# Kernel optimization log

Hardware: AMD Instinct MI355X
Metric: run time of the kernel (lower is better)

Reference implementation:

```python
import jax, jax.numpy as jnp
import numpy as np

B, S, E, H = 2, 2048, 1024, 16
DH = E // H


def setup_inputs() -> dict:
    key = jax.random.key(0)
    ks = jax.random.split(key, 9)
    s = 1.0 / np.sqrt(E)
    return {
        "queries": jax.random.normal(ks[0], (B, S, E), dtype=jnp.float32),
        "keys": jax.random.normal(ks[1], (B, S, E), dtype=jnp.float32),
        "values": jax.random.normal(ks[2], (B, S, E), dtype=jnp.float32),
        "mask": jax.random.randint(ks[3], (B, 1, 1, S), 0, 2, dtype=jnp.int32),
        "Wq": jax.random.normal(ks[4], (E, E), dtype=jnp.float32) * s,
        "Wk": jax.random.normal(ks[5], (E, E), dtype=jnp.float32) * s,
        "Wv": jax.random.normal(ks[6], (E, E), dtype=jnp.float32) * s,
        "Wo": jax.random.normal(ks[7], (E, E), dtype=jnp.float32) * s,
        "bo": jax.random.normal(ks[8], (E,), dtype=jnp.float32) * s,
    }


def reference(queries, keys, values, mask, Wq, Wk, Wv, Wo, bo):
    n, d_q, _ = queries.shape
    d_k = keys.shape[1]
    # Linear projections (torch Linear: x @ W.T), then split into heads
    q = (queries @ Wq.T).reshape(n, d_q, H, DH)
    k = (keys @ Wk.T).reshape(n, d_k, H, DH)
    v = (values @ Wv.T).reshape(n, d_k, H, DH)
    # [n, H, d_q, d_k] attention scores
    energy = jnp.einsum("nqhd,nkhd->nhqk", q, k)
    energy = jnp.where(mask == 0, jnp.float32(-1e20), energy)
    # NOTE: original scales by sqrt(key seq length), not head dim -- kept faithful
    attn = jax.nn.softmax(energy / jnp.sqrt(jnp.float32(d_k)), axis=3)
    out = jnp.einsum("nhql,nlhd->nqhd", attn, v).reshape(n, d_q, E)
    return out @ Wo.T + bo
```

## Files before the change

kernel.cpp:

```cpp
#include <hip/hip_runtime.h>
#include <hip/hip_bf16.h>

#define BB 2
#define SS 2048
#define EE 1024
#define HH 16
#define DHH 64

using bf16x8 = __attribute__((ext_vector_type(8))) __bf16;
using f32x4  = __attribute__((ext_vector_type(4))) float;
using f32x16 = __attribute__((ext_vector_type(16))) float;
using uint2v = __attribute__((ext_vector_type(2))) unsigned int;

#if __has_builtin(__builtin_amdgcn_exp2f)
#define EXP2(x) __builtin_amdgcn_exp2f(x)
#else
#define EXP2(x) __exp2f(x)
#endif

__device__ int g_nkeep[2];

static __device__ __forceinline__ unsigned short f2bf(float f) {
    unsigned int u = __float_as_uint(f);
    u += 0x7FFFu + ((u >> 16) & 1u);
    return (unsigned short)(u >> 16);
}

static __device__ __forceinline__ unsigned int pk2bf(float lo, float hi) {
    union { __hip_bfloat162 h2; unsigned int u; } c;
    c.h2 = __float22bfloat162_rn(float2{lo, hi});
    return c.u;
}

static __device__ __forceinline__ void async_load16(const void* g, void* l) {
    __builtin_amdgcn_global_load_lds(
        (const __attribute__((address_space(1))) unsigned int*)g,
        (__attribute__((address_space(3))) unsigned int*)l, 16, 0, 0);
}

__global__ void cvt_kernel(const float* __restrict__ W0, const float* __restrict__ W1,
                           const float* __restrict__ W2, const float* __restrict__ W3,
                           const int* __restrict__ mask,
                           unsigned short* __restrict__ Wb,
                           int* __restrict__ srcTab)
{
    const int z = blockIdx.y;
    if (z == 4) {
        if (blockIdx.x >= 2) return;
        __shared__ int wsum[4];
        const int b    = blockIdx.x;
        const int tid  = threadIdx.x;
        const int lane = tid & 63;
        const int wave = tid >> 6;

        const int base = tid * 8;
        int v[8]; int run = 0;
        #pragma unroll
        for (int i = 0; i < 8; i++) { v[i] = (mask[b * SS + base + i] != 0) ? 1 : 0; run += v[i]; }

        int inc = run;
        #pragma unroll
        for (int d = 1; d < 64; d <<= 1) {
            int n = __shfl_up(inc, d, 64);
            if (lane >= d) inc += n;
        }
        if (lane == 63) wsum[wave] = inc;

        #pragma unroll
        for (int i = 0; i < 8; i++) srcTab[b * SS + base + i] = -1;
        __syncthreads();

        const int nkeep = wsum[0] + wsum[1] + wsum[2] + wsum[3];
        if (tid == 0) g_nkeep[b] = nkeep;

        int r = inc - run;
        #pragma unroll
        for (int w = 0; w < 4; w++) if (w < wave) r += wsum[w];
        #pragma unroll
        for (int i = 0; i < 8; i++) {
            if (v[i]) { srcTab[b * SS + r] = base + i; r++; }
        }
        return;
    }

    const float* src = (z == 0) ? W0 : (z == 1) ? W1 : (z == 2) ? W2 : W3;
    unsigned short* dst = Wb + (size_t)z * 1048576;
    const size_t base = (size_t)blockIdx.x * 2048 + (size_t)threadIdx.x * 8;
    const float4 f0 = *(const float4*)(src + base);
    const float4 f1 = *(const float4*)(src + base + 4);
    uint4 p;
    p.x = pk2bf(f0.x, f0.y); p.y = pk2bf(f0.z, f0.w);
    p.z = pk2bf(f1.x, f1.y); p.w = pk2bf(f1.z, f1.w);
    *(uint4*)(dst + base) = p;
}

template<int MT, int NT, bool BF16OUT, int AMODE>
__global__ __launch_bounds__(256, 3)
void gemm_xwt(const unsigned short* __restrict__ Xb0, const unsigned short* __restrict__ Xb1,
              const unsigned short* __restrict__ Xb2,
              const float* __restrict__ Xf0, const float* __restrict__ Xf1,
              const float* __restrict__ Xf2, const int* __restrict__ srcTab,
              const unsigned short* __restrict__ W0, const unsigned short* __restrict__ W1,
              const unsigned short* __restrict__ W2,
              void* __restrict__ Y0, void* __restrict__ Y1, void* __restrict__ Y2,
              const float* __restrict__ bias, int M, int N, int K,
              float s0, float s1, float s2)
{
    constexpr int BK = 32;
    constexpr int NI = MT / 32;
    constexpr int NJ = NT / 32;
    constexpr int LPS0 = MT / 64 + NT / 64;
    __shared__ __align__(16) unsigned short As[3][MT * BK];
    __shared__ __align__(16) unsigned short Bs[3][NT * BK];

    const int z = blockIdx.z;
    const unsigned short* __restrict__ W = (z == 0) ? W0 : ((z == 1) ? W1 : W2);
    void* __restrict__ Y                 = (z == 0) ? Y0 : ((z == 1) ? Y1 : Y2);
    const float ysc                      = (z == 0) ? s0 : ((z == 1) ? s1 : s2);

    const int tid  = threadIdx.x;
    const int lane = tid & 63;
    const int wave = tid >> 6;
    const int wm   = (wave >> 1) * (MT / 2);
    const int wn   = (wave & 1) * (NT / 2);

    const unsigned gx  = gridDim.x;
    const unsigned lin = blockIdx.x + gx * blockIdx.y;
    const unsigned k8  = lin & 7u;
    const unsigned j   = lin >> 3;
    const int m0 = (int)(k8 + (j / gx) * 8u) * MT;
    const int n0 = (int)(j % gx) * NT;

    if (AMODE == 1 && z > 0) {
        const int bb = m0 >> 11;
        if ((m0 & 2047) >= g_nkeep[bb]) return;
    }

    const int l16  = lane & 15;
    const int quad = lane >> 4;

    const int arow = lane >> 2;
    const int akc  = ((lane & 3) ^ ((lane >> 3) & 3)) * 8;
    const int rchunk = (quad ^ ((l16 >> 1) & 3)) * 8;
    const int awc  = ((lane & 3) ^ ((arow >> 1) & 3)) * 8;

    f32x4 acc[NI][NJ];
    #pragma unroll
    for (int i = 0; i < NI; i++)
        #pragma unroll
        for (int j2 = 0; j2 < NJ; j2++) acc[i][j2] = f32x4{0.f, 0.f, 0.f, 0.f};

    auto stageB = [&](int k0, int buf) {
        #pragma unroll
        for (int j2 = 0; j2 < NT / 64; j2++) {
            const int rr = wave * (NT / 4) + j2 * 16;
            async_load16(W + (size_t)(n0 + rr + arow) * K + k0 + akc, Bs[buf] + rr * BK);
        }
    };

    auto compute = [&](int buf) {
        bf16x8 afrag[NI], bfrag[NJ];
        #pragma unroll
        for (int ii = 0; ii < NI; ii++)
            afrag[ii] = *(const bf16x8*)(As[buf] + (wm + ii * 16 + l16) * BK + rchunk);
        #pragma unroll
        for (int j2 = 0; j2 < NJ; j2++)
            bfrag[j2] = *(const bf16x8*)(Bs[buf] + (wn + j2 * 16 + l16) * BK + rchunk);
        #pragma unroll
        for (int ii = 0; ii < NI; ii++)
            #pragma unroll
            for (int j2 = 0; j2 < NJ; j2++)
                acc[ii][j2] = __builtin_amdgcn_mfma_f32_16x16x32_bf16(afrag[ii], bfrag[j2], acc[ii][j2], 0, 0, 0);
    };

    const int niter = K / BK;

    if constexpr (AMODE == 0) {
        const unsigned short* __restrict__ X = (z == 0) ? Xb0 : ((z == 1) ? Xb1 : Xb2);
        auto stageA0 = [&](int k0, int buf) {
            #pragma unroll
            for (int j2 = 0; j2 < MT / 64; j2++) {
                const int rr = wave * (MT / 4) + j2 * 16;
                async_load16(X + (size_t)(m0 + rr + arow) * K + k0 + akc, As[buf] + rr * BK);
            }
        };
        stageB(0, 0); stageA0(0, 0);
        stageB(BK, 1); stageA0(BK, 1);
        int cur = 0;
        for (int i = 0; i < niter; i++) {
            if (i + 1 < niter) {
                if constexpr (LPS0 == 4)      asm volatile("s_waitcnt vmcnt(4)" ::: "memory");
                else if constexpr (LPS0 == 3) asm volatile("s_waitcnt vmcnt(3)" ::: "memory");
                else                          asm volatile("s_waitcnt vmcnt(2)" ::: "memory");
            } else {
                asm volatile("s_waitcnt vmcnt(0)" ::: "memory");
            }
            __builtin_amdgcn_s_barrier();
            if (i + 2 < niter) {
                const int nb = (cur >= 1) ? cur - 1 : 2;
                stageB((i + 2) * BK, nb); stageA0((i + 2) * BK, nb);
            }
            compute(cur);
            cur = (cur < 2) ? cur + 1 : 0;
        }
    } else {
        const float* __restrict__ XF = (z == 0) ? Xf0 : ((z == 1) ? Xf1 : Xf2);
        const int bb   = m0 >> 11;
        const int mloc = m0 & 2047;

        const float* aptr[2];
        bool azero[2];
        #pragma unroll
        for (int j2 = 0; j2 < 2; j2++) {
            const int rloc = wave * (MT / 4) + j2 * 16 + arow;
            int grow;
            if (z == 0) {
                grow = m0 + rloc; azero[j2] = false;
            } else {
                const int s = srcTab[bb * SS + mloc + rloc];
                azero[j2] = (s < 0);
                grow = bb * SS + (azero[j2] ? 0 : s);
            }
            aptr[j2] = XF + (size_t)grow * K + (lane & 3) * 8;
        }

        float4 aS0[4], aS1[4];
        #define STAGE_A(k0, S)                                                \
            { _Pragma("unroll")                                               \
              for (int j2 = 0; j2 < 2; j2++) {                                \
                  S[j2 * 2]     = *(const float4*)(aptr[j2] + (k0));          \
                  S[j2 * 2 + 1] = *(const float4*)(aptr[j2] + (k0) + 4);      \
              } }
        #define WRITE_A(buf, S)                                               \
            { _Pragma("unroll")                                               \
              for (int j2 = 0; j2 < 2; j2++) {                                \
                  uint4 w;                                                    \
                  w.x = pk2bf(S[j2*2].x, S[j2*2].y);                          \
                  w.y = pk2bf(S[j2*2].z, S[j2*2].w);                          \
                  w.z = pk2bf(S[j2*2+1].x, S[j2*2+1].y);                      \
                  w.w = pk2bf(S[j2*2+1].z, S[j2*2+1].w);                      \
                  if (azero[j2]) w = uint4{0, 0, 0, 0};                       \
                  const int rr = wave * (MT / 4) + j2 * 16 + arow;            \
                  *(uint4*)(As[buf] + rr * BK + awc) = w;                     \
              } }

        STAGE_A(0, aS0);
        STAGE_A(BK, aS1);
        stageB(0, 0);
        asm volatile("s_waitcnt vmcnt(6)" ::: "memory");
        WRITE_A(0, aS0);
        STAGE_A(2 * BK, aS0);
        stageB(BK, 1);
        asm volatile("s_waitcnt lgkmcnt(0)" ::: "memory");
        asm volatile("s_waitcnt vmcnt(6)" ::: "memory");
        __builtin_amdgcn_s_barrier();

        for (int i = 0; i < niter; i += 2) {
            if (i + 1 < niter) WRITE_A((i + 1) % 3, aS1);
            if (i + 3 < niter) STAGE_A((i + 3) * BK, aS1);
            if (i + 2 < niter) stageB((i + 2) * BK, (i + 2) % 3);
            compute(i % 3);
            asm volatile("s_waitcnt lgkmcnt(0)" ::: "memory");
            if (i + 3 < niter) asm volatile("s_waitcnt vmcnt(6)" ::: "memory");
            else               asm volatile("s_waitcnt vmcnt(0)" ::: "memory");
            __builtin_amdgcn_s_barrier();

            if (i + 2 < niter) WRITE_A((i + 2) % 3, aS0);
            if (i + 4 < niter) STAGE_A((i + 4) * BK, aS0);
            if (i + 3 < niter) stageB((i + 3) * BK, (i + 3) % 3);
            compute((i + 1) % 3);
            if (i + 2 < niter) {
                asm volatile("s_waitcnt lgkmcnt(0)" ::: "memory");
                if (i + 4 < niter) asm volatile("s_waitcnt vmcnt(6)" ::: "memory");
                else               asm volatile("s_waitcnt vmcnt(0)" ::: "memory");
                __builtin_amdgcn_s_barrier();
            }
        }
        #undef STAGE_A
        #undef WRITE_A
    }

    if (BF16OUT && z == 2) {
        #pragma unroll
        for (int i = 0; i < NI; i++) {
            #pragma unroll
            for (int j2 = 0; j2 < NJ; j2++) {
                const int row  = m0 + wm + i * 16 + quad * 4;
                const int bb2  = row >> 11;
                const int slot = row & 2047;
                const int col  = n0 + wn + j2 * 16 + l16;
                uint2 pck;
                pck.x = pk2bf(acc[i][j2][0], acc[i][j2][1]);
                pck.y = pk2bf(acc[i][j2][2], acc[i][j2][3]);
                *(uint2*)((unsigned short*)Y + ((size_t)(bb2 * EE + col)) * SS + slot) = pck;
            }
        }
    } else {
        #pragma unroll
        for (int i = 0; i < NI; i++) {
            #pragma unroll
            for (int j2 = 0; j2 < NJ; j2++) {
                #pragma unroll
                for (int r = 0; r < 4; r++) {
                    const int row = m0 + wm + i * 16 + quad * 4 + r;
                    const int col = n0 + wn + j2 * 16 + l16;
                    const float v = acc[i][j2][r];
                    if (BF16OUT) {
                        ((unsigned short*)Y)[(size_t)row * N + col] = f2bf(v * ysc);
                    } else {
                        ((float*)Y)[(size_t)row * N + col] = v + bias[col];
                    }
                }
            }
        }
    }
}

__global__ __launch_bounds__(256, 2)
void attn_kernel(const unsigned short* __restrict__ Qb,
                 const unsigned short* __restrict__ Kc,
                 const unsigned short* __restrict__ Vtc,
                 const int* __restrict__ mask,
                 unsigned short* __restrict__ AO)
{
    constexpr int LDK = 68;
    constexpr int LDV = 68;
    __shared__ __align__(16) unsigned short Ks[64 * LDK];
    __shared__ __align__(16) unsigned short Vs[64 * LDV];
    __shared__ float Lsum[4][32];
    __shared__ int nk_s;

    const int tid  = threadIdx.x;
    const int lane = tid & 63;
    const int wave = tid >> 6;
    const int l32  = lane & 31;
    const int hi   = lane >> 5;

    const int linear = blockIdx.x;
    const int bh     = (linear & 7) * 4 + ((linear >> 3) & 3);
    const int qblk   = linear >> 5;
    const int b  = bh >> 4;
    const int h  = bh & 15;
    const int q0 = qblk * 128 + wave * 32;

    if (tid == 0) nk_s = 0;
    __syncthreads();
    {
        int cnt = 0;
        #pragma unroll
        for (int i = 0; i < 8; i++) cnt += (mask[b * SS + tid * 8 + i] != 0) ? 1 : 0;
        #pragma unroll
        for (int d = 32; d >= 1; d >>= 1) cnt += __shfl_xor(cnt, d, 64);
        if (lane == 0) atomicAdd(&nk_s, cnt);
    }
    __syncthreads();
    const int nkeep  = nk_s;
    const int ntiles = (nkeep + 63) >> 6;

    bf16x8 qf[4];
    {
        const unsigned short* qptr = Qb + (size_t)(b * SS + q0 + l32) * EE + h * DHH + hi * 8;
        #pragma unroll
        for (int t = 0; t < 4; t++) qf[t] = *(const bf16x8*)(qptr + t * 16);
    }

    float lsum = 0.f;
    f32x16 o_acc[2];
    #pragma unroll
    for (int d = 0; d < 2; d++)
        #pragma unroll
        for (int r = 0; r < 16; r++) o_acc[d][r] = 0.f;

    const int srow = tid >> 2;
    const int sc   = (tid & 3) * 16;

    uint4 kr0, kr1, vr0, vr1;
    auto gload = [&](int t0) {
        const unsigned short* kg = Kc + (size_t)(b * SS + t0 + srow) * EE + h * DHH + sc;
        kr0 = *(const uint4*)(kg);
        kr1 = *(const uint4*)(kg + 8);
        const unsigned short* vg = Vtc + (size_t)(b * EE + h * DHH + srow) * SS + t0 + sc;
        vr0 = *(const uint4*)(vg);
        vr1 = *(const uint4*)(vg + 8);
    };
    gload(0);

    for (int it = 0; it < ntiles; it++) {
        const int t0 = it * 64;
        __syncthreads();
        *(uint4*)(Ks + srow * LDK + sc)     = kr0;
        *(uint4*)(Ks + srow * LDK + sc + 8) = kr1;
        *(uint4*)(Vs + srow * LDV + sc)     = vr0;
        *(uint4*)(Vs + srow * LDV + sc + 8) = vr1;
        __syncthreads();

        if (it + 1 < ntiles) gload(t0 + 64);

        const bool full = (t0 + 64 <= nkeep);

        #pragma unroll
        for (int blk = 0; blk < 2; blk++) {
            f32x16 s;
            __builtin_amdgcn_s_setprio(1);
            {
                bf16x8 kf = *(const bf16x8*)(Ks + (blk * 32 + l32) * LDK + hi * 8);
                f32x16 z;
                #pragma unroll
                for (int r = 0; r < 16; r++) z[r] = 0.f;
                s = __builtin_amdgcn_mfma_f32_32x32x16_bf16(kf, qf[0], z, 0, 0, 0);
            }
            #pragma unroll
            for (int t = 1; t < 4; t++) {
                bf16x8 kf = *(const bf16x8*)(Ks + (blk * 32 + l32) * LDK + t * 16 + hi * 8);
                s = __builtin_amdgcn_mfma_f32_32x32x16_bf16(kf, qf[t], s, 0, 0, 0);
            }
            __builtin_amdgcn_s_setprio(0);

            float p[16];
            #pragma unroll
            for (int r = 0; r < 16; r++) p[r] = EXP2(s[r]);
            if (!full) {
                const int keyb = t0 + blk * 32 + 4 * hi;
                #pragma unroll
                for (int r = 0; r < 16; r++)
                    if (keyb + ((r & 3) + 8 * (r >> 2)) >= nkeep) p[r] = 0.f;
            }
            #pragma unroll
            for (int r = 0; r < 16; r += 4)
                lsum += ((p[r] + p[r + 1]) + (p[r + 2] + p[r + 3]));

            const unsigned int u0 = pk2bf(p[0],  p[1]);
            const unsigned int u1 = pk2bf(p[2],  p[3]);
            const unsigned int u2 = pk2bf(p[4],  p[5]);
            const unsigned int u3 = pk2bf(p[6],  p[7]);
            const unsigned int u4 = pk2bf(p[8],  p[9]);
            const unsigned int u5 = pk2bf(p[10], p[11]);
            const unsigned int u6 = pk2bf(p[12], p[13]);
            const unsigned int u7 = pk2bf(p[14], p[15]);
            const uint2v s02 = __builtin_amdgcn_permlane32_swap(u0, u2, false, false);
            const uint2v s13 = __builtin_amdgcn_permlane32_swap(u1, u3, false, false);
            const uint2v s46 = __builtin_amdgcn_permlane32_swap(u4, u6, false, false);
            const uint2v s57 = __builtin_amdgcn_permlane32_swap(u5, u7, false, false);

            union { unsigned int u[4]; bf16x8 v; } pa0, pa1;
            pa0.u[0] = s02.x; pa0.u[1] = s13.x; pa0.u[2] = s02.y; pa0.u[3] = s13.y;
            pa1.u[0] = s46.x; pa1.u[1] = s57.x; pa1.u[2] = s46.y; pa1.u[3] = s57.y;

            __builtin_amdgcn_s_setprio(1);
            #pragma unroll
            for (int kc = 0; kc < 2; kc++) {
                const bf16x8 pav = (kc == 0) ? pa0.v : pa1.v;
                #pragma unroll
                for (int dblk = 0; dblk < 2; dblk++) {
                    bf16x8 vf = *(const bf16x8*)(Vs + (dblk * 32 + l32) * LDV + blk * 32 + kc * 16 + hi * 8);
                    o_acc[dblk] = __builtin_amdgcn_mfma_f32_32x32x16_bf16(pav, vf, o_acc[dblk], 0, 0, 0);
                }
            }
            __builtin_amdgcn_s_setprio(0);
        }
    }

    {
        float ls = lsum;
        ls += __shfl_xor(ls, 32, 64);
        Lsum[wave][l32] = 1.0f / ls;
    }
    __builtin_amdgcn_s_waitcnt(0xC07F);

    #pragma unroll
    for (int r = 0; r < 16; r++) {
        const int qr = (r & 3) + 8 * (r >> 2) + 4 * hi;
        const float rl = Lsum[wave][qr];
        const size_t orow = (size_t)(b * SS + q0 + qr) * EE + h * DHH + l32;
        AO[orow]      = f2bf(o_acc[0][r] * rl);
        AO[orow + 32] = f2bf(o_acc[1][r] * rl);
    }
}

extern "C" void kernel_launch(void* const* d_in, const int* in_sizes, int n_in,
                              void* d_out, int out_size, void* d_ws, size_t ws_size,
                              hipStream_t stream)
{
    (void)in_sizes; (void)n_in; (void)out_size; (void)ws_size;
    const float* queries = (const float*)d_in[0];
    const float* keys    = (const float*)d_in[1];
    const float* values  = (const float*)d_in[2];
    const int*   mask    = (const int*)d_in[3];
    const float* Wq      = (const float*)d_in[4];
    const float* Wk      = (const float*)d_in[5];
    const float* Wv      = (const float*)d_in[6];
    const float* Wo      = (const float*)d_in[7];
    const float* bo      = (const float*)d_in[8];

    const size_t NE = (size_t)BB * SS * EE;
    const size_t WE = (size_t)EE * EE;

    unsigned short* Wb  = (unsigned short*)d_ws;
    unsigned short* Qb  = Wb + 4 * WE;
    unsigned short* Kc  = Qb + NE;
    unsigned short* Vtc = Kc + NE;
    unsigned short* AOb = Vtc + NE;

    int* srcTab = (int*)d_out;

    const int M = BB * SS, N = EE, K = EE;
    const float qscale = 0.022097086912079608f * 1.4426950408889634f;

    cvt_kernel<<<dim3(512, 5), 256, 0, stream>>>(
        Wq, Wk, Wv, Wo, mask, Wb, srcTab);

    dim3 gproj(N / 128, M / 128, 3);
    gemm_xwt<128, 128, true, 1><<<gproj, 256, 0, stream>>>(
        nullptr, nullptr, nullptr,
        queries, keys, values, srcTab,
        Wb, Wb + WE, Wb + 2 * WE,
        (void*)Qb, (void*)Kc, (void*)Vtc, nullptr, M, N, K,
        qscale, 1.0f, 1.0f);

    attn_kernel<<<dim3(512), 256, 0, stream>>>(Qb, Kc, Vtc, mask, AOb);

    dim3 gout(N / 64, M / 64, 1);
    gemm_xwt<64, 64, false, 0><<<gout, 256, 0, stream>>>(
        AOb, AOb, AOb,
        nullptr, nullptr, nullptr, nullptr,
        Wb + 3 * WE, Wb + 3 * WE, Wb + 3 * WE,
        d_out, d_out, d_out, bo, M, N, K, 1.0f, 1.0f, 1.0f);
}
```

Before: 205.4 us.

## Use intra-block split-K with 512 threads for output projection GEMM

The output projection GEMM now uses 128x64 tiles with 512 threads, where two groups of four waves each handle half of the K dimension with separate triple-buffered LDS stages. At the end the halves are reduced through shared memory. The block-to-tile swizzle is also changed so that the eight-block groups stride across M. The aim is more waves per tile for latency hiding and better reuse of the larger A tile. The cost is extra LDS use, a reduction step and an additional barrier.

```diff
diff --git a/kernel.cpp b/kernel.cpp
--- a/kernel.cpp
+++ b/kernel.cpp
@@ -94,8 +94,8 @@
     *(uint4*)(dst + base) = p;
 }
 
-template<int MT, int NT, bool BF16OUT, int AMODE>
-__global__ __launch_bounds__(256, 3)
+template<int MT, int NT, bool BF16OUT, int AMODE, int NTH = 256>
+__global__ __launch_bounds__(NTH, NTH == 256 ? 3 : 4)
 void gemm_xwt(const unsigned short* __restrict__ Xb0, const unsigned short* __restrict__ Xb1,
               const unsigned short* __restrict__ Xb2,
               const float* __restrict__ Xf0, const float* __restrict__ Xf1,
@@ -109,9 +109,11 @@
     constexpr int BK = 32;
     constexpr int NI = MT / 32;
     constexpr int NJ = NT / 32;
+    constexpr bool SPLITK = (NTH == 512);
+    constexpr int NBUF = SPLITK ? 6 : 3;
     constexpr int LPS0 = MT / 64 + NT / 64;
-    __shared__ __align__(16) unsigned short As[3][MT * BK];
-    __shared__ __align__(16) unsigned short Bs[3][NT * BK];
+    __shared__ __align__(16) unsigned short As[NBUF][MT * BK];
+    __shared__ __align__(16) unsigned short Bs[NBUF][NT * BK];
 
     const int z = blockIdx.z;
     const unsigned short* __restrict__ W = (z == 0) ? W0 : ((z == 1) ? W1 : W2);
@@ -121,14 +123,17 @@
     const int tid  = threadIdx.x;
     const int lane = tid & 63;
     const int wave = tid >> 6;
-    const int wm   = (wave >> 1) * (MT / 2);
-    const int wn   = (wave & 1) * (NT / 2);
+    const int kh   = SPLITK ? (wave >> 2) : 0;
+    const int wq   = SPLITK ? (wave & 3) : wave;
+    const int wm   = (wq >> 1) * (MT / 2);
+    const int wn   = (wq & 1) * (NT / 2);
 
     const unsigned gx  = gridDim.x;
+    const unsigned gy  = gridDim.y;
     const unsigned lin = blockIdx.x + gx * blockIdx.y;
     const unsigned k8  = lin & 7u;
     const unsigned j   = lin >> 3;
-    const int m0 = (int)(k8 + (j / gx) * 8u) * MT;
+    const int m0 = (int)(k8 * (gy >> 3) + j / gx) * MT;
     const int n0 = (int)(j % gx) * NT;
 
     if (AMODE == 1 && z > 0) {
@@ -150,22 +155,22 @@
         #pragma unroll
         for (int j2 = 0; j2 < NJ; j2++) acc[i][j2] = f32x4{0.f, 0.f, 0.f, 0.f};
 
-    auto stageB = [&](int k0, int buf) {
+    auto stageB = [&](int k0, int bufAbs) {
         #pragma unroll
         for (int j2 = 0; j2 < NT / 64; j2++) {
-            const int rr = wave * (NT / 4) + j2 * 16;
-            async_load16(W + (size_t)(n0 + rr + arow) * K + k0 + akc, Bs[buf] + rr * BK);
+            const int rr = wq * (NT / 4) + j2 * 16;
+            async_load16(W + (size_t)(n0 + rr + arow) * K + k0 + akc, Bs[bufAbs] + rr * BK);
         }
     };
 
-    auto compute = [&](int buf) {
+    auto compute = [&](int bufAbs) {
         bf16x8 afrag[NI], bfrag[NJ];
         #pragma unroll
         for (int ii = 0; ii < NI; ii++)
-            afrag[ii] = *(const bf16x8*)(As[buf] + (wm + ii * 16 + l16) * BK + rchunk);
+            afrag[ii] = *(const bf16x8*)(As[bufAbs] + (wm + ii * 16 + l16) * BK + rchunk);
         #pragma unroll
         for (int j2 = 0; j2 < NJ; j2++)
-            bfrag[j2] = *(const bf16x8*)(Bs[buf] + (wn + j2 * 16 + l16) * BK + rchunk);
+            bfrag[j2] = *(const bf16x8*)(Bs[bufAbs] + (wn + j2 * 16 + l16) * BK + rchunk);
         #pragma unroll
         for (int ii = 0; ii < NI; ii++)
             #pragma unroll
@@ -173,19 +178,21 @@
                 acc[ii][j2] = __builtin_amdgcn_mfma_f32_16x16x32_bf16(afrag[ii], bfrag[j2], acc[ii][j2], 0, 0, 0);
     };
 
-    const int niter = K / BK;
-
     if constexpr (AMODE == 0) {
         const unsigned short* __restrict__ X = (z == 0) ? Xb0 : ((z == 1) ? Xb1 : Xb2);
-        auto stageA0 = [&](int k0, int buf) {
+        auto stageA0 = [&](int k0, int bufAbs) {
             #pragma unroll
             for (int j2 = 0; j2 < MT / 64; j2++) {
-                const int rr = wave * (MT / 4) + j2 * 16;
-                async_load16(X + (size_t)(m0 + rr + arow) * K + k0 + akc, As[buf] + rr * BK);
+                const int rr = wq * (MT / 4) + j2 * 16;
+                async_load16(X + (size_t)(m0 + rr + arow) * K + k0 + akc, As[bufAbs] + rr * BK);
             }
         };
-        stageB(0, 0); stageA0(0, 0);
-        stageB(BK, 1); stageA0(BK, 1);
+        const int kbase = SPLITK ? kh * (K / 2) : 0;
+        const int niter = (SPLITK ? K / 2 : K) / BK;
+        const int bof   = kh * 3;
+
+        stageB(kbase, bof + 0); stageA0(kbase, bof + 0);
+        stageB(kbase + BK, bof + 1); stageA0(kbase + BK, bof + 1);
         int cur = 0;
         for (int i = 0; i < niter; i++) {
             if (i + 1 < niter) {
@@ -198,12 +205,37 @@
             __builtin_amdgcn_s_barrier();
             if (i + 2 < niter) {
                 const int nb = (cur >= 1) ? cur - 1 : 2;
-                stageB((i + 2) * BK, nb); stageA0((i + 2) * BK, nb);
-            }
-            compute(cur);
+                stageB(kbase + (i + 2) * BK, bof + nb); stageA0(kbase + (i + 2) * BK, bof + nb);
+            }
+            compute(bof + cur);
             cur = (cur < 2) ? cur + 1 : 0;
         }
+
+        if constexpr (SPLITK) {
+            __syncthreads();
+            float* red = (float*)&As[0][0];
+            const int slot = ((wq * 64 + lane) * (NI * NJ * 4));
+            if (kh == 1) {
+                #pragma unroll
+                for (int i = 0; i < NI; i++)
+                    #pragma unroll
+                    for (int j2 = 0; j2 < NJ; j2++)
+                        #pragma unroll
+                        for (int r = 0; r < 4; r++)
+                            red[slot + (i * NJ + j2) * 4 + r] = acc[i][j2][r];
+            }
+            __syncthreads();
+            if (kh == 1) return;
+            #pragma unroll
+            for (int i = 0; i < NI; i++)
+                #pragma unroll
+                for (int j2 = 0; j2 < NJ; j2++)
+                    #pragma unroll
+                    for (int r = 0; r < 4; r++)
+                        acc[i][j2][r] += red[slot + (i * NJ + j2) * 4 + r];
+        }
     } else {
+        const int niter = K / BK;
         const float* __restrict__ XF = (z == 0) ? Xf0 : ((z == 1) ? Xf1 : Xf2);
         const int bb   = m0 >> 11;
         const int mloc = m0 & 2047;
@@ -212,7 +244,7 @@
         bool azero[2];
         #pragma unroll
         for (int j2 = 0; j2 < 2; j2++) {
-            const int rloc = wave * (MT / 4) + j2 * 16 + arow;
+            const int rloc = wq * (MT / 4) + j2 * 16 + arow;
             int grow;
             if (z == 0) {
                 grow = m0 + rloc; azero[j2] = false;
@@ -240,7 +272,7 @@
                   w.z = pk2bf(S[j2*2+1].x, S[j2*2+1].y);                      \
                   w.w = pk2bf(S[j2*2+1].z, S[j2*2+1].w);                      \
                   if (azero[j2]) w = uint4{0, 0, 0, 0};                       \
-                  const int rr = wave * (MT / 4) + j2 * 16 + arow;            \
+                  const int rr = wq * (MT / 4) + j2 * 16 + arow;              \
                   *(uint4*)(As[buf] + rr * BK + awc) = w;                     \
               } }
 
@@ -510,7 +542,7 @@
         Wq, Wk, Wv, Wo, mask, Wb, srcTab);
 
     dim3 gproj(N / 128, M / 128, 3);
-    gemm_xwt<128, 128, true, 1><<<gproj, 256, 0, stream>>>(
+    gemm_xwt<128, 128, true, 1, 256><<<gproj, 256, 0, stream>>>(
         nullptr, nullptr, nullptr,
         queries, keys, values, srcTab,
         Wb, Wb + WE, Wb + 2 * WE,
@@ -519,8 +551,8 @@
 
     attn_kernel<<<dim3(512), 256, 0, stream>>>(Qb, Kc, Vtc, mask, AOb);
 
-    dim3 gout(N / 64, M / 64, 1);
-    gemm_xwt<64, 64, false, 0><<<gout, 256, 0, stream>>>(
+    dim3 gout(N / 64, M / 128, 1);
+    gemm_xwt<128, 64, false, 0, 512><<<gout, 512, 0, stream>>>(
         AOb, AOb, AOb,
         nullptr, nullptr, nullptr, nullptr,
         Wb + 3 * WE, Wb + 3 * WE, Wb + 3 * WE,
```

Result: no change. 207.0 us (+0.8%).
